# Performance work log

Hardware: AMD Instinct MI355X
Metric: run time of the kernel (lower is better)

Reference implementation:

```python
import jax, jax.numpy as jnp
import numpy as np

P = 128      # fingerprint length
H = 512      # hidden size
QE = 100_000 # atoms per element type
E = 3        # element types
Q = E * QE   # total atoms
N = 1000     # images in batch
NNZ = 8_000_000  # nnz of sparse fprime matrix [P*Q, 3*Q]


def _mlp(x, w0, b0, w1, b1, w2, b2):
    h = jnp.tanh(x @ w0 + b0)
    h = jnp.tanh(h @ w1 + b1)
    return h @ w2 + b2  # [Qe, 1]


def setup_inputs() -> dict:
    key = jax.random.key(0)
    ks = jax.random.split(key, 32)
    inp = {}
    k = 0
    s0 = 1.0 / np.sqrt(P)
    s1 = 1.0 / np.sqrt(H)
    for e in range(E):
        inp[f"x{e}"] = jax.random.normal(ks[k], (QE, P), jnp.float32); k += 1
        inp[f"idx{e}"] = jax.random.randint(ks[k], (QE,), 0, N); k += 1
        inp[f"w{e}0"] = jax.random.uniform(ks[k], (P, H), jnp.float32, -s0, s0); k += 1
        inp[f"b{e}0"] = jnp.zeros((H,), jnp.float32)
        inp[f"w{e}1"] = jax.random.uniform(ks[k], (H, H), jnp.float32, -s1, s1); k += 1
        inp[f"b{e}1"] = jnp.zeros((H,), jnp.float32)
        inp[f"w{e}2"] = jax.random.uniform(ks[k], (H, 1), jnp.float32, -s1, s1); k += 1
        inp[f"b{e}2"] = jnp.zeros((1,), jnp.float32)
    inp["rearange"] = jax.random.permutation(ks[k], Q); k += 1
    inp["fp_rows"] = jax.random.randint(ks[k], (NNZ,), 0, Q * P); k += 1
    inp["fp_cols"] = jax.random.randint(ks[k], (NNZ,), 0, 3 * Q); k += 1
    inp["fp_vals"] = jax.random.normal(ks[k], (NNZ,), jnp.float32) * 0.01; k += 1
    return inp


def reference(x0, x1, x2,
              w00, b00, w01, b01, w02, b02,
              w10, b10, w11, b11, w12, b12,
              w20, b20, w21, b21, w22, b22,
              fp_vals, idx0, idx1, idx2, rearange, fp_rows, fp_cols):
    xs = [x0, x1, x2]
    idxs = [idx0, idx1, idx2]
    params = [(w00, b00, w01, b01, w02, b02),
              (w10, b10, w11, b11, w12, b12),
              (w20, b20, w21, b21, w22, b22)]
    energy = jnp.zeros((N, 1), jnp.float32)
    dEs = []
    for e in range(E):  # loop over fixed small set of element types
        out = _mlp(xs[e], *params[e])           # [QE, 1] atomwise energies
        energy = energy.at[idxs[e]].add(out)    # index_add_ into per-image energy
        # dE/dFP: per-atom gradient of its scalar energy wrt its fingerprint
        g = jax.grad(lambda x, p=params[e]: _mlp(x, *p).sum())(xs[e])  # [QE, P]
        dEs.append(g)
    dE = jnp.concatenate(dEs, axis=0)           # [Q, P]
    idx_all = jnp.concatenate(idxs)             # [Q]
    # torch nonzero(boolean.t()) ordering == stable sort by image index
    ordered = jnp.argsort(idx_all, stable=True)
    dE = dE[ordered][rearange].reshape(-1)      # [P*Q] fingerprint order
    # force = -fprimes.T @ dE  (sparse COO: fprimes is [P*Q, 3*Q])
    contrib = fp_vals * dE[fp_rows]
    force = -jax.ops.segment_sum(contrib, fp_cols, num_segments=3 * Q)
    force = force.reshape(-1, 3)                # [Q, 3]
    return energy, force
```

## Files before the change

kernel.cpp:

```cpp
#include <hip/hip_runtime.h>

#define P_   128
#define H_   512
#define QE_  100000
#define Q_   300000
#define NIMG 1000
#define NNZ_ 8000000
#define NC_  1172
#define ROWS 64
#define NBLK 1563

typedef __attribute__((ext_vector_type(8))) short bf16x8;
typedef __attribute__((ext_vector_type(4))) float f32x4;

__device__ __forceinline__ ushort f2bf(float f) {
  union { float f; unsigned u; } v; v.f = f;
  unsigned r = v.u + 0x7FFF + ((v.u >> 16) & 1);
  return (ushort)(r >> 16);
}
__device__ __forceinline__ float bf2f(ushort h) {
  union { unsigned u; float f; } v; v.u = ((unsigned)h) << 16;
  return v.f;
}
__device__ __forceinline__ float fast_tanh(float x) {
  float e = __expf(2.f * x);
  return 1.f - 2.f / (e + 1.f);
}

struct ElemPtrs {
  const float* x; const int* idx;
  const ushort *w0t, *w0b, *w1t, *w1b;
  const float *b0, *b1, *w2, *b2;
};
struct AllPtrs { ElemPtrs e[3]; };

template <int K, int LDB>
__device__ __forceinline__ void gphase(const ushort* __restrict__ Alds,
                                       const ushort* __restrict__ Bt,
                                       int fr, int fk, f32x4 acc[4][4]) {
  const ushort* bp[4];
#pragma unroll
  for (int j = 0; j < 4; ++j) bp[j] = Bt + (size_t)(j * 16 + fr) * LDB + fk;
  const ushort* ap[4];
  int xr[4];
#pragma unroll
  for (int i = 0; i < 4; ++i) {
    int row = i * 16 + fr;
    ap[i] = Alds + row * K;
    xr[i] = (row & 7) << 3;
  }
  bf16x8 ac[4], bc[4];
#pragma unroll
  for (int i = 0; i < 4; ++i) ac[i] = *(const bf16x8*)(ap[i] + (fk ^ xr[i]));
#pragma unroll
  for (int j = 0; j < 4; ++j) bc[j] = *(const bf16x8*)(bp[j]);
#pragma unroll
  for (int kt = 0; kt < K; kt += 32) {
    bf16x8 an[4], bn[4];
    if (kt + 32 < K) {
#pragma unroll
      for (int j = 0; j < 4; ++j) bn[j] = *(const bf16x8*)(bp[j] + kt + 32);
#pragma unroll
      for (int i = 0; i < 4; ++i)
        an[i] = *(const bf16x8*)(ap[i] + (((kt + 32) + fk) ^ xr[i]));
    }
#pragma unroll
    for (int i = 0; i < 4; ++i)
#pragma unroll
      for (int j = 0; j < 4; ++j)
        acc[i][j] = __builtin_amdgcn_mfma_f32_16x16x32_bf16(ac[i], bc[j], acc[i][j], 0, 0, 0);
    if (kt + 32 < K) {
#pragma unroll
      for (int i = 0; i < 4; ++i) ac[i] = an[i];
#pragma unroll
      for (int j = 0; j < 4; ++j) bc[j] = bn[j];
    }
  }
}

template <int K, int LDB>
__device__ __forceinline__ void gphaseD(const ushort* __restrict__ Alds,
                                        const ushort* __restrict__ Bt,
                                        int rbase, int fr, int fk, f32x4 acc[4]) {
  const ushort* bp[4];
#pragma unroll
  for (int j = 0; j < 4; ++j) bp[j] = Bt + (size_t)(j * 16 + fr) * LDB + fk;
  const int row = rbase + fr;
  const ushort* ap = Alds + row * K;
  const int xr = (row & 7) << 3;
  bf16x8 ac = *(const bf16x8*)(ap + (fk ^ xr));
  bf16x8 bc[4];
#pragma unroll
  for (int j = 0; j < 4; ++j) bc[j] = *(const bf16x8*)(bp[j]);
#pragma unroll
  for (int kt = 0; kt < K; kt += 32) {
    bf16x8 an, bn[4];
    if (kt + 32 < K) {
#pragma unroll
      for (int j = 0; j < 4; ++j) bn[j] = *(const bf16x8*)(bp[j] + kt + 32);
      an = *(const bf16x8*)(ap + (((kt + 32) + fk) ^ xr));
    }
#pragma unroll
    for (int j = 0; j < 4; ++j)
      acc[j] = __builtin_amdgcn_mfma_f32_16x16x32_bf16(ac, bc[j], acc[j], 0, 0, 0);
    if (kt + 32 < K) {
      ac = an;
#pragma unroll
      for (int j = 0; j < 4; ++j) bc[j] = bn[j];
    }
  }
}

__global__ __launch_bounds__(512) void k_fused(AllPtrs ps, ushort* __restrict__ dEb,
                                               float* __restrict__ energy) {
  __shared__ ushort bufA[ROWS * H_];
  __shared__ ushort bufB[ROWS * H_];
  __shared__ ushort bufX[ROWS * P_];
  __shared__ float b0l[H_], b1l[H_], w2l[H_];
  __shared__ float e_lds[ROWS];

  const int bid = blockIdx.x;
  const int e = bid / NBLK;
  const int blk = bid - e * NBLK;
  const int base = blk * ROWS;
  const int Mloc = min(ROWS, QE_ - base);
  const ElemPtrs EP = ps.e[e];

  const int tid = threadIdx.x;
  const int w = tid >> 6;
  const int lane = tid & 63;
  const int fr = lane & 15;
  const int fk = (lane >> 4) * 8;
  const int q4 = (lane >> 4) * 4;

  b0l[tid] = EP.b0[tid];
  b1l[tid] = EP.b1[tid];
  w2l[tid] = EP.w2[tid];
  if (tid < ROWS) e_lds[tid] = 0.f;
#pragma unroll
  for (int s = 0; s < 2; ++s) {
    int q = tid * 2 + s;
    int row = q >> 4, c = q & 15;
    ushort ov[8];
    if (row < Mloc) {
      const float* src = EP.x + (size_t)(base + row) * P_ + c * 8;
      float4 v0 = *(const float4*)src;
      float4 v1 = *(const float4*)(src + 4);
      ov[0] = f2bf(v0.x); ov[1] = f2bf(v0.y); ov[2] = f2bf(v0.z); ov[3] = f2bf(v0.w);
      ov[4] = f2bf(v1.x); ov[5] = f2bf(v1.y); ov[6] = f2bf(v1.z); ov[7] = f2bf(v1.w);
    } else {
#pragma unroll
      for (int t = 0; t < 8; ++t) ov[t] = 0;
    }
    int idx = (row * P_ + c * 8) ^ ((row & 7) << 3);
    *(bf16x8*)(bufX + idx) = *(bf16x8*)ov;
  }
  __syncthreads();

  {
    f32x4 acc[4][4] = {};
    gphase<P_, P_>(bufX, EP.w0t + (size_t)(w * 64) * P_, fr, fk, acc);
#pragma unroll
    for (int j = 0; j < 4; ++j) {
      int col = w * 64 + j * 16 + fr;
      float bj = b0l[col];
#pragma unroll
      for (int i = 0; i < 4; ++i)
#pragma unroll
        for (int r = 0; r < 4; ++r) {
          int row = i * 16 + q4 + r;
          bufA[(row * H_ + col) ^ ((row & 7) << 3)] = f2bf(fast_tanh(acc[i][j][r] + bj));
        }
    }
  }
  __syncthreads();

  {
    f32x4 acc[4][4] = {};
    gphase<H_, H_>(bufA, EP.w1t + (size_t)(w * 64) * H_, fr, fk, acc);
    float ep[4][4] = {};
#pragma unroll
    for (int j = 0; j < 4; ++j) {
      int col = w * 64 + j * 16 + fr;
      float bj = b1l[col], wj = w2l[col];
#pragma unroll
      for (int i = 0; i < 4; ++i)
#pragma unroll
        for (int r = 0; r < 4; ++r) {
          int row = i * 16 + q4 + r;
          float h = fast_tanh(acc[i][j][r] + bj);
          ep[i][r] += h * wj;
          bufB[(row * H_ + col) ^ ((row & 7) << 3)] = f2bf(wj * (1.f - h * h));
        }
    }
#pragma unroll
    for (int i = 0; i < 4; ++i)
#pragma unroll
      for (int r = 0; r < 4; ++r) {
        float v = ep[i][r];
        v += __shfl_xor(v, 1, 64); v += __shfl_xor(v, 2, 64);
        v += __shfl_xor(v, 4, 64); v += __shfl_xor(v, 8, 64);
        if (fr == 0) atomicAdd(&e_lds[i * 16 + q4 + r], v);
      }
  }
  __syncthreads();
  if (tid < Mloc) atomicAdd(&energy[EP.idx[base + tid]], e_lds[tid] + EP.b2[0]);

  {
    f32x4 acc[4][4] = {};
    gphase<H_, H_>(bufB, EP.w1b + (size_t)(w * 64) * H_, fr, fk, acc);
    __syncthreads();
#pragma unroll
    for (int j = 0; j < 4; ++j) {
      int col = w * 64 + j * 16 + fr;
#pragma unroll
      for (int i = 0; i < 4; ++i)
#pragma unroll
        for (int r = 0; r < 4; ++r) {
          int row = i * 16 + q4 + r;
          int sidx = (row * H_ + col) ^ ((row & 7) << 3);
          float h = bf2f(bufA[sidx]);
          bufB[sidx] = f2bf(acc[i][j][r] * (1.f - h * h));
        }
    }
  }
  __syncthreads();

  {
    f32x4 acc4[4] = {};
    const int rbase = (w & 3) * 16;
    const int cbase = (w >> 2) * 64;
    gphaseD<H_, H_>(bufB, EP.w0b + (size_t)cbase * H_, rbase, fr, fk, acc4);
#pragma unroll
    for (int j = 0; j < 4; ++j) {
      int col = cbase + j * 16 + fr;
#pragma unroll
      for (int r = 0; r < 4; ++r)
        bufX[(rbase + q4 + r) * P_ + col] = f2bf(acc4[j][r]);
    }
  }
  __syncthreads();
  {
    const size_t rowOff = (size_t)e * QE_ + base;
#pragma unroll
    for (int s = 0; s < 2; ++s) {
      int q = tid * 2 + s;
      int row = q >> 4, c = q & 15;
      if (row < Mloc)
        *(bf16x8*)(dEb + (rowOff + row) * P_ + c * 8) = *(const bf16x8*)(bufX + q * 8);
    }
  }
}

__global__ __launch_bounds__(256) void k_cvt(const float* __restrict__ src,
                                             ushort* __restrict__ dst, int n) {
  int i = (blockIdx.x * 256 + threadIdx.x) * 4;
  if (i < n) {
    float4 v = *(const float4*)(src + i);
    ushort o[4] = {f2bf(v.x), f2bf(v.y), f2bf(v.z), f2bf(v.w)};
    *(uint2*)(dst + i) = *(uint2*)o;
  }
}
__global__ __launch_bounds__(256) void k_cvt_t(const float* __restrict__ src,
                                               ushort* __restrict__ dst, int R, int C) {
  int i = blockIdx.x * 256 + threadIdx.x;
  if (i < R * C) {
    int c = i / R, r = i - c * R;
    dst[i] = f2bf(src[(size_t)r * C + c]);
  }
}

__device__ __forceinline__ int atom_key(int gi, const int* i0, const int* i1, const int* i2) {
  return gi < QE_ ? i0[gi] : (gi < 2 * QE_ ? i1[gi - QE_] : i2[gi - 2 * QE_]);
}

__global__ __launch_bounds__(256) void k_hist(
    const int* __restrict__ i0, const int* __restrict__ i1, const int* __restrict__ i2,
    int* __restrict__ chunkHist) {
  __shared__ int h[NIMG];
  for (int i = threadIdx.x; i < NIMG; i += 256) h[i] = 0;
  __syncthreads();
  int gi = blockIdx.x * 256 + threadIdx.x;
  if (gi < Q_) atomicAdd(&h[atom_key(gi, i0, i1, i2)], 1);
  __syncthreads();
  for (int i = threadIdx.x; i < NIMG; i += 256)
    chunkHist[(size_t)blockIdx.x * NIMG + i] = h[i];
}

__global__ __launch_bounds__(256) void k_scanchunks(int* __restrict__ chunkHist,
                                                    int* __restrict__ binTotals) {
  __shared__ int s[256];
  __shared__ int carry;
  const int b = blockIdx.x;
  if (threadIdx.x == 0) carry = 0;
  __syncthreads();
  for (int c0 = 0; c0 < NC_; c0 += 256) {
    int c = c0 + threadIdx.x;
    int v = (c < NC_) ? chunkHist[(size_t)c * NIMG + b] : 0;
    s[threadIdx.x] = v;
    __syncthreads();
#pragma unroll
    for (int off = 1; off < 256; off <<= 1) {
      int t = (threadIdx.x >= off) ? s[threadIdx.x - off] : 0;
      __syncthreads();
      s[threadIdx.x] += t;
      __syncthreads();
    }
    int incl = s[threadIdx.x];
    int base = carry;
    __syncthreads();
    if (c < NC_) chunkHist[(size_t)c * NIMG + b] = base + incl - v;
    if (threadIdx.x == 255) carry = base + s[255];
    __syncthreads();
  }
  if (threadIdx.x == 0) binTotals[b] = carry;
}

__global__ void k_binoffsets(const int* __restrict__ binTotals, int* __restrict__ binOffset) {
  if (threadIdx.x == 0 && blockIdx.x == 0) {
    int acc = 0;
    for (int b = 0; b < NIMG; b++) { binOffset[b] = acc; acc += binTotals[b]; }
  }
}

__global__ __launch_bounds__(256) void k_scatter(
    const int* __restrict__ i0, const int* __restrict__ i1, const int* __restrict__ i2,
    const int* __restrict__ chunkHist, const int* __restrict__ binOffset,
    int* __restrict__ ordered) {
  __shared__ int keys[256];
  int gi = blockIdx.x * 256 + threadIdx.x;
  int key = (gi < Q_) ? atom_key(gi, i0, i1, i2) : -1;
  keys[threadIdx.x] = key;
  __syncthreads();
  if (gi < Q_) {
    int rank = 0;
    for (int j = 0; j < threadIdx.x; j++) rank += (keys[j] == key) ? 1 : 0;
    ordered[binOffset[key] + chunkHist[(size_t)blockIdx.x * NIMG + key] + rank] = gi;
  }
}

__global__ __launch_bounds__(256) void k_force(
    const int* __restrict__ fp_rows, const int* __restrict__ fp_cols,
    const float* __restrict__ fp_vals, const int* __restrict__ rearange,
    const int* __restrict__ ordered, const ushort* __restrict__ dEb,
    float* __restrict__ force) {
  int n = blockIdx.x * 256 + threadIdx.x;
  if (n >= NNZ_) return;
  int r = fp_rows[n];
  int src = ordered[rearange[r >> 7]];
  float contrib = fp_vals[n] * bf2f(dEb[(size_t)src * P_ + (r & 127)]);
  atomicAdd(&force[fp_cols[n]], -contrib);
}

extern "C" void kernel_launch(void* const* d_in, const int* in_sizes, int n_in,
                              void* d_out, int out_size, void* d_ws, size_t ws_size,
                              hipStream_t stream) {
  const float *x[3], *w0[3], *b0[3], *w1[3], *b1[3], *w2[3], *b2[3];
  const int* idx[3];
  for (int e = 0; e < 3; e++) {
    const int o = e * 8;
    x[e]   = (const float*)d_in[o + 0];
    idx[e] = (const int*)  d_in[o + 1];
    w0[e]  = (const float*)d_in[o + 2];
    b0[e]  = (const float*)d_in[o + 3];
    w1[e]  = (const float*)d_in[o + 4];
    b1[e]  = (const float*)d_in[o + 5];
    w2[e]  = (const float*)d_in[o + 6];
    b2[e]  = (const float*)d_in[o + 7];
  }
  const int*   rearange = (const int*)  d_in[24];
  const int*   fp_rows  = (const int*)  d_in[25];
  const int*   fp_cols  = (const int*)  d_in[26];
  const float* fp_vals  = (const float*)d_in[27];
  float* out = (float*)d_out;

  const size_t W_PER_E = 65536 + 65536 + 262144 + 262144;
  ushort* dEb   = (ushort*)d_ws;
  ushort* wbase = dEb + (size_t)Q_ * P_;
  int* chunkHist = (int*)(wbase + 3 * W_PER_E);
  int* binTotals = chunkHist + (size_t)NC_ * NIMG;
  int* binOffset = binTotals + 1024;
  int* ordered   = binOffset + 1024;

  hipMemsetAsync(d_out, 0, (size_t)out_size * sizeof(float), stream);

  AllPtrs ps;
  for (int e = 0; e < 3; e++) {
    ushort* w0t = wbase + e * W_PER_E;
    ushort* w0b = w0t + 65536;
    ushort* w1t = w0b + 65536;
    ushort* w1b = w1t + 262144;
    k_cvt_t<<<(65536 + 255) / 256, 256, 0, stream>>>(w0[e], w0t, 128, 512);
    k_cvt<<<(65536 / 4 + 255) / 256, 256, 0, stream>>>(w0[e], w0b, 65536);
    k_cvt_t<<<(262144 + 255) / 256, 256, 0, stream>>>(w1[e], w1t, 512, 512);
    k_cvt<<<(262144 / 4 + 255) / 256, 256, 0, stream>>>(w1[e], w1b, 262144);
    ps.e[e] = ElemPtrs{x[e], idx[e], w0t, w0b, w1t, w1b, b0[e], b1[e], w2[e], b2[e]};
  }

  k_fused<<<3 * NBLK, 512, 0, stream>>>(ps, dEb, out);

  k_hist<<<NC_, 256, 0, stream>>>(idx[0], idx[1], idx[2], chunkHist);
  k_scanchunks<<<NIMG, 256, 0, stream>>>(chunkHist, binTotals);
  k_binoffsets<<<1, 64, 0, stream>>>(binTotals, binOffset);
  k_scatter<<<NC_, 256, 0, stream>>>(idx[0], idx[1], idx[2], chunkHist, binOffset, ordered);
  k_force<<<(NNZ_ + 255) / 256, 256, 0, stream>>>(fp_rows, fp_cols, fp_vals, rearange,
                                                  ordered, dEb, out + NIMG);
}
```

Measured before the change: 2.055 ms.

## Shrink fused MLP tile to 48 rows and reuse smaller LDS buffers for occupancy

Reduces the per-block row tile from 64 to 48 and replaces the two full 64x512 LDS buffers plus the X buffer with one 48x512 buffer and one 48x256 half buffer. Half of the second-layer backward gradient is stashed in registers while the other half is consumed, and the dh1 GEMM is split into two K=256 passes. The last GEMM is redistributed so every wave does 16 output columns. The GEMM loops now load A fragments from LDS inside the iteration instead of prefetching them, and launch bounds request 4 blocks per CU. The goal is to lower LDS use so more blocks fit per CU. The cost is more blocks, extra barriers and register pressure from the stash.

```diff
diff --git a/kernel.cpp b/kernel.cpp
--- a/kernel.cpp
+++ b/kernel.cpp
@@ -7,8 +7,8 @@
 #define NIMG 1000
 #define NNZ_ 8000000
 #define NC_  1172
-#define ROWS 64
-#define NBLK 1563
+#define ROWS 48
+#define NBLK 2084
 
 typedef __attribute__((ext_vector_type(8))) short bf16x8;
 typedef __attribute__((ext_vector_type(4))) float f32x4;
@@ -34,88 +34,74 @@
 };
 struct AllPtrs { ElemPtrs e[3]; };
 
-template <int K, int LDB>
-__device__ __forceinline__ void gphase(const ushort* __restrict__ Alds,
-                                       const ushort* __restrict__ Bt,
-                                       int fr, int fk, f32x4 acc[4][4]) {
-  const ushort* bp[4];
-#pragma unroll
-  for (int j = 0; j < 4; ++j) bp[j] = Bt + (size_t)(j * 16 + fr) * LDB + fk;
-  const ushort* ap[4];
-  int xr[4];
-#pragma unroll
-  for (int i = 0; i < 4; ++i) {
+template <int MI, int K, int ASTR>
+__device__ __forceinline__ void gphase4(const ushort* __restrict__ Alds,
+                                        const ushort* const* __restrict__ bp,
+                                        int fr, int fk, f32x4 (*acc)[4]) {
+  int xr[MI]; const ushort* ap[MI];
+#pragma unroll
+  for (int i = 0; i < MI; ++i) {
     int row = i * 16 + fr;
-    ap[i] = Alds + row * K;
+    ap[i] = Alds + row * ASTR;
     xr[i] = (row & 7) << 3;
   }
-  bf16x8 ac[4], bc[4];
-#pragma unroll
-  for (int i = 0; i < 4; ++i) ac[i] = *(const bf16x8*)(ap[i] + (fk ^ xr[i]));
+  bf16x8 bc[4];
 #pragma unroll
   for (int j = 0; j < 4; ++j) bc[j] = *(const bf16x8*)(bp[j]);
 #pragma unroll
   for (int kt = 0; kt < K; kt += 32) {
-    bf16x8 an[4], bn[4];
+    bf16x8 bn[4];
     if (kt + 32 < K) {
 #pragma unroll
       for (int j = 0; j < 4; ++j) bn[j] = *(const bf16x8*)(bp[j] + kt + 32);
-#pragma unroll
-      for (int i = 0; i < 4; ++i)
-        an[i] = *(const bf16x8*)(ap[i] + (((kt + 32) + fk) ^ xr[i]));
-    }
-#pragma unroll
-    for (int i = 0; i < 4; ++i)
+    }
+    bf16x8 ac[MI];
+#pragma unroll
+    for (int i = 0; i < MI; ++i)
+      ac[i] = *(const bf16x8*)(ap[i] + ((kt + fk) ^ xr[i]));
+#pragma unroll
+    for (int i = 0; i < MI; ++i)
 #pragma unroll
       for (int j = 0; j < 4; ++j)
         acc[i][j] = __builtin_amdgcn_mfma_f32_16x16x32_bf16(ac[i], bc[j], acc[i][j], 0, 0, 0);
     if (kt + 32 < K) {
 #pragma unroll
-      for (int i = 0; i < 4; ++i) ac[i] = an[i];
-#pragma unroll
       for (int j = 0; j < 4; ++j) bc[j] = bn[j];
     }
   }
 }
 
-template <int K, int LDB>
-__device__ __forceinline__ void gphaseD(const ushort* __restrict__ Alds,
-                                        const ushort* __restrict__ Bt,
-                                        int rbase, int fr, int fk, f32x4 acc[4]) {
-  const ushort* bp[4];
-#pragma unroll
-  for (int j = 0; j < 4; ++j) bp[j] = Bt + (size_t)(j * 16 + fr) * LDB + fk;
-  const int row = rbase + fr;
-  const ushort* ap = Alds + row * K;
-  const int xr = (row & 7) << 3;
-  bf16x8 ac = *(const bf16x8*)(ap + (fk ^ xr));
-  bf16x8 bc[4];
-#pragma unroll
-  for (int j = 0; j < 4; ++j) bc[j] = *(const bf16x8*)(bp[j]);
+template <int MI, int K, int ASTR>
+__device__ __forceinline__ void gphase1(const ushort* __restrict__ Alds,
+                                        const ushort* __restrict__ bp0,
+                                        int fr, int fk, f32x4* acc) {
+  int xr[MI]; const ushort* ap[MI];
+#pragma unroll
+  for (int i = 0; i < MI; ++i) {
+    int row = i * 16 + fr;
+    ap[i] = Alds + row * ASTR;
+    xr[i] = (row & 7) << 3;
+  }
+  bf16x8 bc = *(const bf16x8*)(bp0);
 #pragma unroll
   for (int kt = 0; kt < K; kt += 32) {
-    bf16x8 an, bn[4];
-    if (kt + 32 < K) {
-#pragma unroll
-      for (int j = 0; j < 4; ++j) bn[j] = *(const bf16x8*)(bp[j] + kt + 32);
-      an = *(const bf16x8*)(ap + (((kt + 32) + fk) ^ xr));
-    }
-#pragma unroll
-    for (int j = 0; j < 4; ++j)
-      acc[j] = __builtin_amdgcn_mfma_f32_16x16x32_bf16(ac, bc[j], acc[j], 0, 0, 0);
-    if (kt + 32 < K) {
-      ac = an;
-#pragma unroll
-      for (int j = 0; j < 4; ++j) bc[j] = bn[j];
-    }
-  }
-}
-
-__global__ __launch_bounds__(512) void k_fused(AllPtrs ps, ushort* __restrict__ dEb,
-                                               float* __restrict__ energy) {
-  __shared__ ushort bufA[ROWS * H_];
-  __shared__ ushort bufB[ROWS * H_];
-  __shared__ ushort bufX[ROWS * P_];
+    bf16x8 bn;
+    if (kt + 32 < K) bn = *(const bf16x8*)(bp0 + kt + 32);
+    bf16x8 ac[MI];
+#pragma unroll
+    for (int i = 0; i < MI; ++i)
+      ac[i] = *(const bf16x8*)(ap[i] + ((kt + fk) ^ xr[i]));
+#pragma unroll
+    for (int i = 0; i < MI; ++i)
+      acc[i] = __builtin_amdgcn_mfma_f32_16x16x32_bf16(ac[i], bc, acc[i], 0, 0, 0);
+    if (kt + 32 < K) bc = bn;
+  }
+}
+
+__global__ __launch_bounds__(512, 4) void k_fused(AllPtrs ps, ushort* __restrict__ dEb,
+                                                  float* __restrict__ energy) {
+  __shared__ ushort buf[ROWS * H_];
+  __shared__ ushort half[ROWS * 256];
   __shared__ float b0l[H_], b1l[H_], w2l[H_];
   __shared__ float e_lds[ROWS];
 
@@ -139,62 +125,87 @@
   if (tid < ROWS) e_lds[tid] = 0.f;
 #pragma unroll
   for (int s = 0; s < 2; ++s) {
-    int q = tid * 2 + s;
-    int row = q >> 4, c = q & 15;
-    ushort ov[8];
-    if (row < Mloc) {
-      const float* src = EP.x + (size_t)(base + row) * P_ + c * 8;
-      float4 v0 = *(const float4*)src;
-      float4 v1 = *(const float4*)(src + 4);
-      ov[0] = f2bf(v0.x); ov[1] = f2bf(v0.y); ov[2] = f2bf(v0.z); ov[3] = f2bf(v0.w);
-      ov[4] = f2bf(v1.x); ov[5] = f2bf(v1.y); ov[6] = f2bf(v1.z); ov[7] = f2bf(v1.w);
-    } else {
-#pragma unroll
-      for (int t = 0; t < 8; ++t) ov[t] = 0;
-    }
-    int idx = (row * P_ + c * 8) ^ ((row & 7) << 3);
-    *(bf16x8*)(bufX + idx) = *(bf16x8*)ov;
+    int q = tid + s * 512;
+    if (q < ROWS * 16) {
+      int row = q >> 4, c = q & 15;
+      ushort ov[8];
+      if (row < Mloc) {
+        const float* src = EP.x + (size_t)(base + row) * P_ + c * 8;
+        float4 v0 = *(const float4*)src;
+        float4 v1 = *(const float4*)(src + 4);
+        ov[0] = f2bf(v0.x); ov[1] = f2bf(v0.y); ov[2] = f2bf(v0.z); ov[3] = f2bf(v0.w);
+        ov[4] = f2bf(v1.x); ov[5] = f2bf(v1.y); ov[6] = f2bf(v1.z); ov[7] = f2bf(v1.w);
+      } else {
+#pragma unroll
+        for (int t = 0; t < 8; ++t) ov[t] = 0;
+      }
+      int idx = (row * P_ + c * 8) ^ ((row & 7) << 3);
+      *(bf16x8*)(half + idx) = *(bf16x8*)ov;
+    }
   }
   __syncthreads();
 
   {
-    f32x4 acc[4][4] = {};
-    gphase<P_, P_>(bufX, EP.w0t + (size_t)(w * 64) * P_, fr, fk, acc);
+    f32x4 acc[3][4] = {};
+    const ushort* bp[4];
+#pragma unroll
+    for (int j = 0; j < 4; ++j)
+      bp[j] = EP.w0t + (size_t)(w * 64 + j * 16 + fr) * P_ + fk;
+    gphase4<3, P_, P_>(half, bp, fr, fk, acc);
 #pragma unroll
     for (int j = 0; j < 4; ++j) {
       int col = w * 64 + j * 16 + fr;
       float bj = b0l[col];
 #pragma unroll
-      for (int i = 0; i < 4; ++i)
+      for (int i = 0; i < 3; ++i)
 #pragma unroll
         for (int r = 0; r < 4; ++r) {
           int row = i * 16 + q4 + r;
-          bufA[(row * H_ + col) ^ ((row & 7) << 3)] = f2bf(fast_tanh(acc[i][j][r] + bj));
+          buf[(row * H_ + col) ^ ((row & 7) << 3)] = f2bf(fast_tanh(acc[i][j][r] + bj));
         }
     }
   }
   __syncthreads();
 
+  unsigned stash[3][2][2];
   {
-    f32x4 acc[4][4] = {};
-    gphase<H_, H_>(bufA, EP.w1t + (size_t)(w * 64) * H_, fr, fk, acc);
-    float ep[4][4] = {};
+    f32x4 acc[3][4] = {};
+    const ushort* bp[4];
 #pragma unroll
     for (int j = 0; j < 4; ++j) {
-      int col = w * 64 + j * 16 + fr;
+      int col = (j < 2) ? (w * 32 + j * 16 + fr) : (256 + w * 32 + (j - 2) * 16 + fr);
+      bp[j] = EP.w1t + (size_t)col * H_ + fk;
+    }
+    gphase4<3, H_, H_>(buf, bp, fr, fk, acc);
+    float ep[3][4] = {};
+#pragma unroll
+    for (int j = 0; j < 4; ++j) {
+      int kidx = w * 32 + (j & 1) * 16 + fr;
+      int col = (j < 2) ? kidx : (256 + kidx);
       float bj = b1l[col], wj = w2l[col];
-#pragma unroll
-      for (int i = 0; i < 4; ++i)
+      ushort dv[4];
+#pragma unroll
+      for (int i = 0; i < 3; ++i) {
 #pragma unroll
         for (int r = 0; r < 4; ++r) {
-          int row = i * 16 + q4 + r;
           float h = fast_tanh(acc[i][j][r] + bj);
           ep[i][r] += h * wj;
-          bufB[(row * H_ + col) ^ ((row & 7) << 3)] = f2bf(wj * (1.f - h * h));
+          dv[r] = f2bf(wj * (1.f - h * h));
         }
-    }
-#pragma unroll
-    for (int i = 0; i < 4; ++i)
+        if (j < 2) {
+#pragma unroll
+          for (int r = 0; r < 4; ++r) {
+            int row = i * 16 + q4 + r;
+            half[(row * 256 + kidx) ^ ((row & 7) << 3)] = dv[r];
+          }
+        } else {
+          stash[i][j - 2][0] = (unsigned)dv[0] | ((unsigned)dv[1] << 16);
+          stash[i][j - 2][1] = (unsigned)dv[2] | ((unsigned)dv[3] << 16);
+        }
+      }
+    }
+#pragma unroll
+    for (int i = 0; i < 3; ++i)
 #pragma unroll
       for (int r = 0; r < 4; ++r) {
         float v = ep[i][r];
@@ -207,47 +218,68 @@
   if (tid < Mloc) atomicAdd(&energy[EP.idx[base + tid]], e_lds[tid] + EP.b2[0]);
 
   {
-    f32x4 acc[4][4] = {};
-    gphase<H_, H_>(bufB, EP.w1b + (size_t)(w * 64) * H_, fr, fk, acc);
+    f32x4 acc[3][4] = {};
+    const ushort* bp[4];
+#pragma unroll
+    for (int j = 0; j < 4; ++j)
+      bp[j] = EP.w1b + (size_t)(w * 64 + j * 16 + fr) * H_ + fk;
+    gphase4<3, 256, 256>(half, bp, fr, fk, acc);
     __syncthreads();
+#pragma unroll
+    for (int i = 0; i < 3; ++i)
+#pragma unroll
+      for (int jj = 0; jj < 2; ++jj) {
+        int kidx = w * 32 + jj * 16 + fr;
+#pragma unroll
+        for (int r = 0; r < 4; ++r) {
+          int row = i * 16 + q4 + r;
+          half[(row * 256 + kidx) ^ ((row & 7) << 3)] =
+              (ushort)(stash[i][jj][r >> 1] >> ((r & 1) * 16));
+        }
+      }
+    __syncthreads();
+    const ushort* bp2[4];
+#pragma unroll
+    for (int j = 0; j < 4; ++j) bp2[j] = bp[j] + 256;
+    gphase4<3, 256, 256>(half, bp2, fr, fk, acc);
 #pragma unroll
     for (int j = 0; j < 4; ++j) {
       int col = w * 64 + j * 16 + fr;
 #pragma unroll
-      for (int i = 0; i < 4; ++i)
+      for (int i = 0; i < 3; ++i)
 #pragma unroll
         for (int r = 0; r < 4; ++r) {
           int row = i * 16 + q4 + r;
           int sidx = (row * H_ + col) ^ ((row & 7) << 3);
-          float h = bf2f(bufA[sidx]);
-          bufB[sidx] = f2bf(acc[i][j][r] * (1.f - h * h));
+          float m = bf2f(buf[sidx]);
+          buf[sidx] = f2bf(acc[i][j][r] * (1.f - m * m));
         }
     }
   }
   __syncthreads();
 
   {
-    f32x4 acc4[4] = {};
-    const int rbase = (w & 3) * 16;
-    const int cbase = (w >> 2) * 64;
-    gphaseD<H_, H_>(bufB, EP.w0b + (size_t)cbase * H_, rbase, fr, fk, acc4);
-#pragma unroll
-    for (int j = 0; j < 4; ++j) {
-      int col = cbase + j * 16 + fr;
+    f32x4 acc[3] = {};
+    const ushort* bp0 = EP.w0b + (size_t)(w * 16 + fr) * H_ + fk;
+    gphase1<3, H_, H_>(buf, bp0, fr, fk, acc);
+    int col = w * 16 + fr;
+#pragma unroll
+    for (int i = 0; i < 3; ++i)
 #pragma unroll
       for (int r = 0; r < 4; ++r)
-        bufX[(rbase + q4 + r) * P_ + col] = f2bf(acc4[j][r]);
-    }
+        half[(i * 16 + q4 + r) * P_ + col] = f2bf(acc[i][r]);
   }
   __syncthreads();
   {
     const size_t rowOff = (size_t)e * QE_ + base;
 #pragma unroll
     for (int s = 0; s < 2; ++s) {
-      int q = tid * 2 + s;
-      int row = q >> 4, c = q & 15;
-      if (row < Mloc)
-        *(bf16x8*)(dEb + (rowOff + row) * P_ + c * 8) = *(const bf16x8*)(bufX + q * 8);
+      int q = tid + s * 512;
+      if (q < ROWS * 16) {
+        int row = q >> 4, c = q & 15;
+        if (row < Mloc)
+          *(bf16x8*)(dEb + (rowOff + row) * P_ + c * 8) = *(const bf16x8*)(half + q * 8);
+      }
     }
   }
 }
```

Result: faster. 1.959 ms (-4.7%).
